# Optimization experiments

Hardware: AMD Instinct MI355X
Metric: run time of the kernel (lower is better)

Reference implementation:

```python
import jax, jax.numpy as jnp
import numpy as np

EPS = 1e-5


def _corner_data(x, cmin, stride, D, H, W):
    # continuous grid indices (x_idx, y_idx, z_idx); index 0 = first voxel center
    idx = (x - cmin[None, :]) / stride[None, :]
    gx, gy, gz = idx[:, 0], idx[:, 1], idx[:, 2]
    x0 = jnp.floor(gx); y0 = jnp.floor(gy); z0 = jnp.floor(gz)
    fx = jnp.clip(gx - x0, 0.0, 1.0)
    fy = jnp.clip(gy - y0, 0.0, 1.0)
    fz = jnp.clip(gz - z0, 0.0, 1.0)
    x0i = x0.astype(jnp.int32); x1i = x0i + 1
    y0i = y0.astype(jnp.int32); y1i = y0i + 1
    z0i = z0.astype(jnp.int32); z1i = z0i + 1
    # 8 trilinear corners, same order as the torch reference
    xs = jnp.stack([x0i, x1i, x0i, x1i, x0i, x1i, x0i, x1i])
    ys = jnp.stack([y0i, y0i, y1i, y1i, y0i, y0i, y1i, y1i])
    zs = jnp.stack([z0i, z0i, z0i, z0i, z1i, z1i, z1i, z1i])
    wx = jnp.stack([1 - fx, fx, 1 - fx, fx, 1 - fx, fx, 1 - fx, fx])
    wy = jnp.stack([1 - fy, 1 - fy, fy, fy, 1 - fy, 1 - fy, fy, fy])
    wz = jnp.stack([1 - fz, 1 - fz, 1 - fz, 1 - fz, fz, fz, fz, fz])
    ws = wx * wy * wz                                    # (8, N)
    valid = (xs >= 0) & (xs < W) & (ys >= 0) & (ys < H) & (zs >= 0) & (zs < D)
    xi = jnp.clip(xs, 0, W - 1)
    yi = jnp.clip(ys, 0, H - 1)
    zi = jnp.clip(zs, 0, D - 1)
    flat = zi * (H * W) + yi * W + xi                    # (8, N) flat voxel index
    return flat, ws * valid.astype(ws.dtype)


def setup_inputs() -> dict:
    key = jax.random.key(0)
    ks = jax.random.split(key, 20)
    N = 200000; B = 4; D = H = W = 64; CG = 64; NC = 128; HID = 128
    h = jax.random.normal(ks[0], (N, NC), jnp.float32)
    x = jax.random.uniform(ks[1], (N, 3), jnp.float32) * 63.0
    grid = jax.random.normal(ks[2], (B, CG, D, H, W), jnp.float32)
    node_batch = jax.random.randint(ks[3], (N,), 0, B, jnp.int32)
    coordinates_min = jnp.zeros((3,), jnp.float32)
    spatial_stride = jnp.ones((3,), jnp.float32)
    s = 0.05
    params = dict(
        w1=jax.random.normal(ks[4], (HID, NC + CG), jnp.float32) * s,
        b1=jax.random.normal(ks[5], (HID,), jnp.float32) * s,
        w2=jax.random.normal(ks[6], (NC, HID), jnp.float32) * s,
        b2=jax.random.normal(ks[7], (NC,), jnp.float32) * s,
        ln_g=1.0 + jax.random.normal(ks[8], (NC,), jnp.float32) * s,
        ln_b=jax.random.normal(ks[9], (NC,), jnp.float32) * s,
        wn2g=jax.random.normal(ks[10], (CG, NC), jnp.float32) * s,
        bn2g=jax.random.normal(ks[11], (CG,), jnp.float32) * s,
        wc1=jax.random.normal(ks[12], (CG, 2 * CG), jnp.float32) * s,
        bc1=jax.random.normal(ks[13], (CG,), jnp.float32) * s,
        wc2=jax.random.normal(ks[14], (CG, CG), jnp.float32) * s,
        bc2=jax.random.normal(ks[15], (CG,), jnp.float32) * s,
        in_g=1.0 + jax.random.normal(ks[16], (CG,), jnp.float32) * s,
        in_b=jax.random.normal(ks[17], (CG,), jnp.float32) * s,
    )
    return dict(h=h, x=x, grid=grid, node_batch=node_batch,
                coordinates_min=coordinates_min, spatial_stride=spatial_stride, **params)


def reference(h, x, grid, node_batch, coordinates_min, spatial_stride,
              w1, b1, w2, b2, ln_g, ln_b, wn2g, bn2g, wc1, bc1, wc2, bc2, in_g, in_b):
    B, Cg, D, H, W = grid.shape
    DHW = D * H * W
    flat, w = _corner_data(x, coordinates_min, spatial_stride, D, H, W)  # (8,N)

    # grid -> node: trilinear gather (== grid_sample, align_corners=True, zeros padding)
    gflat = grid.reshape(B, Cg, DHW).transpose(0, 2, 1)                  # (B,DHW,Cg)
    vals = gflat[node_batch[None, :], flat]                              # (8,N,Cg)
    sampled = jnp.einsum('kn,knc->nc', w, vals)                          # (N,Cg)

    # node MLP + residual + LayerNorm
    z = jnp.concatenate([h, sampled], axis=-1)
    m = jax.nn.silu(z @ w1.T + b1) @ w2.T + b2
    hn = h + m
    mu = hn.mean(-1, keepdims=True)
    var = hn.var(-1, keepdims=True)
    hn = (hn - mu) / jnp.sqrt(var + EPS) * ln_g + ln_b

    # node -> grid: trilinear scatter-add splat of projected features
    proj = hn @ wn2g.T + bn2g                                            # (N,Cg)
    gidx = node_batch[None, :] * DHW + flat                              # (8,N) global flat index
    contrib = w[:, :, None] * proj[None]                                 # (8,N,Cg)
    vol = jnp.zeros((B * DHW, Cg), grid.dtype).at[gidx.reshape(-1)].add(contrib.reshape(-1, Cg))
    splat = vol.reshape(B, D, H, W, Cg).transpose(0, 4, 1, 2, 3)         # (B,Cg,D,H,W)

    # grid MLP (1x1x1 convs) + residual + InstanceNorm (affine)
    cat = jnp.concatenate([grid, splat], axis=1)                         # (B,2Cg,D,H,W)
    g1 = jax.nn.silu(jnp.einsum('bcdhw,oc->bodhw', cat, wc1) + bc1[None, :, None, None, None])
    g2 = jnp.einsum('bcdhw,oc->bodhw', g1, wc2) + bc2[None, :, None, None, None]
    gr = grid + g2
    mu = gr.mean((2, 3, 4), keepdims=True)
    var = gr.var((2, 3, 4), keepdims=True)
    gr = (gr - mu) / jnp.sqrt(var + EPS) * in_g[None, :, None, None, None] + in_b[None, :, None, None, None]
    return hn, gr
```

## Files before the change

### kernel.cpp

```cpp
#include <hip/hip_runtime.h>
#include <hip/hip_fp16.h>
#include <cstdint>

#define NNODES 200000
#define NCH 128
#define NBATCH 4
#define DHW 262144
#define K1 192

#define VOLH_OFF  0ull
#define VOLH_BYTES 134217728ull
#define PART_OFF  134217728ull
#define STAT_OFF  142606336ull
#define NWF_OFF   142608384ull
#define WF_OFF    142706688ull
#define GT_OFF    257931264ull
#define GRH_OFF   392149056ull

typedef _Float16 h2 __attribute__((ext_vector_type(2)));
typedef __fp16  fp16x2 __attribute__((ext_vector_type(2)));
typedef _Float16 f16x8 __attribute__((ext_vector_type(8)));
typedef float f32x4 __attribute__((ext_vector_type(4)));

__device__ __forceinline__ uint32_t pack_h2(float a, float b){
  fp16x2 p = __builtin_amdgcn_cvt_pkrtz(a, b);
  return __builtin_bit_cast(uint32_t, p);
}
__device__ __forceinline__ h2 as_h2(uint32_t w){ return __builtin_bit_cast(h2, w); }
__device__ __forceinline__ float siluf(float a){ return a / (1.f + __expf(-a)); }
__device__ __forceinline__ f32x4 mfma16(uint4 a, uint4 b, f32x4 c){
  return __builtin_amdgcn_mfma_f32_16x16x32_f16(
      __builtin_bit_cast(f16x8, a), __builtin_bit_cast(f16x8, b), c, 0, 0, 0);
}
__device__ __forceinline__ void atomic_pk_add_f16(uint32_t* addr, uint32_t val){
  asm volatile("global_atomic_pk_add_f16 %0, %1, off"
               :: "v"(addr), "v"(val) : "memory");
}

__global__ void fill_kernel(uint4* __restrict__ p, size_t n4)
{
  size_t stride = (size_t)gridDim.x * 256;
  const uint4 z = make_uint4(0u, 0u, 0u, 0u);
  for (size_t i = blockIdx.x * 256 + threadIdx.x; i < n4; i += stride) p[i] = z;
}

__global__ void pack_all(const float* __restrict__ w1, const float* __restrict__ w2,
                         const float* __restrict__ wn2g,
                         const float* __restrict__ wc1, const float* __restrict__ wc2,
                         uint32_t* __restrict__ nwf, uint32_t* __restrict__ wf)
{
  int t = blockIdx.x * 256 + threadIdx.x;
  if (t < 24576) {
    int q = t & 3, lane = (t >> 2) & 63;
    int vl = lane & 15, g = lane >> 4;
    if (t < 12288) {
      int f = t >> 8, s = f % 6, tt = f / 6;
      int o = tt * 16 + vl, k = s * 32 + g * 8 + 2 * q;
      nwf[t] = pack_h2(w1[o * K1 + k], w1[o * K1 + k + 1]);
    } else if (t < 20480) {
      int f = (t - 12288) >> 8, s = f & 3, tt = f >> 2;
      int o = tt * 16 + vl, k = s * 32 + g * 8 + 2 * q;
      nwf[t] = pack_h2(w2[o * 128 + k], w2[o * 128 + k + 1]);
    } else {
      int f = (t - 20480) >> 8, s = f & 3, tt = f >> 2;
      int o = tt * 16 + vl, k = s * 32 + g * 8 + 2 * q;
      nwf[t] = pack_h2(wn2g[o * 128 + k], wn2g[o * 128 + k + 1]);
    }
  } else if (t < 30720) {
    int u = t - 24576;
    if (u < 4096) {
      int q = u & 3, lane = (u >> 2) & 63, f = u >> 8;
      int s = f & 3, tt = f >> 2;
      int o = tt * 16 + (lane & 15);
      int k = s * 32 + (lane >> 4) * 8 + 2 * q;
      wf[u] = pack_h2(wc1[o * 128 + k], wc1[o * 128 + k + 1]);
    } else {
      int uu = u - 4096;
      int q = uu & 3, lane = (uu >> 2) & 63, f = uu >> 8;
      int s = f & 1, tt = f >> 1;
      int o = tt * 16 + (lane & 15);
      int k = s * 32 + (lane >> 4) * 8 + 2 * q;
      wf[u] = pack_h2(wc2[o * 64 + k], wc2[o * 64 + k + 1]);
    }
  }
}

__global__ void transpose_kernel(const float* __restrict__ grid, uint32_t* __restrict__ gt)
{
  __shared__ float tile[64][65];
  int bx = blockIdx.x;
  int b = bx >> 12;
  int dhw0 = (bx & 4095) << 6;
  const float* gbase = grid + ((size_t)b * 64) * DHW + dhw0;
  int c0 = threadIdx.x >> 6, d = threadIdx.x & 63;
  #pragma unroll
  for (int i = 0; i < 16; ++i)
    tile[i * 4 + c0][d] = gbase[(size_t)(i * 4 + c0) * DHW + d];
  __syncthreads();
  uint32_t* tb = gt + ((size_t)b * DHW + dhw0) * 32;
  int p = threadIdx.x & 31, r0 = threadIdx.x >> 5;
  #pragma unroll
  for (int i = 0; i < 8; ++i) {
    int dd = i * 8 + r0;
    tb[(size_t)dd * 32 + p] = pack_h2(tile[2 * p][dd], tile[2 * p + 1][dd]);
  }
}

__launch_bounds__(256, 2)
__global__ void node_fused(const float* __restrict__ h, const float* __restrict__ x,
                           const uint32_t* __restrict__ gridT, const int* __restrict__ nbat,
                           const float* __restrict__ cmin, const float* __restrict__ sstr,
                           const uint32_t* __restrict__ nwf,
                           const float* __restrict__ b1, const float* __restrict__ b2,
                           const float* __restrict__ ln_g, const float* __restrict__ ln_b,
                           const float* __restrict__ bn2g,
                           float* __restrict__ hn_out, uint32_t* __restrict__ volh)
{
  __shared__ __align__(16) uint32_t zt[64][100];
  __shared__ __align__(16) uint32_t g1z[64][68];
  __shared__ float wpart[4][64][2];
  __shared__ float cwS[64][8];
  __shared__ int   cfS[64][8];

  const int tid = threadIdx.x;
  const int lane = tid & 63, w = tid >> 6;
  const int g = lane >> 4, vl = lane & 15;
  const int n0 = blockIdx.x * 64;

  {
    const float c0 = cmin[0], c1 = cmin[1], c2 = cmin[2];
    const float st0 = sstr[0], st1 = sstr[1], st2 = sstr[2];
    int nd = tid & 63, j = tid >> 6;
    int n = n0 + nd;
    float gx = (x[n * 3 + 0] - c0) / st0;
    float gy = (x[n * 3 + 1] - c1) / st1;
    float gz = (x[n * 3 + 2] - c2) / st2;
    float fx0 = floorf(gx), fy0 = floorf(gy), fz0 = floorf(gz);
    float fx = fminf(fmaxf(gx - fx0, 0.f), 1.f);
    float fy = fminf(fmaxf(gy - fy0, 0.f), 1.f);
    float fz = fminf(fmaxf(gz - fz0, 0.f), 1.f);
    int ix0 = (int)fx0, iy0 = (int)fy0, iz0 = (int)fz0;
    int b = nbat[n];
    #pragma unroll
    for (int kk = 0; kk < 2; ++kk) {
      int k = 2 * j + kk;
      int xi = (k & 1) ? ix0 + 1 : ix0;
      int yi = (k & 2) ? iy0 + 1 : iy0;
      int zi = (k & 4) ? iz0 + 1 : iz0;
      float wx = (k & 1) ? fx : 1.f - fx;
      float wy = (k & 2) ? fy : 1.f - fy;
      float wz = (k & 4) ? fz : 1.f - fz;
      bool valid = (xi >= 0) & (xi < 64) & (yi >= 0) & (yi < 64) & (zi >= 0) & (zi < 64);
      int xc = min(max(xi, 0), 63), yc = min(max(yi, 0), 63), zc = min(max(zi, 0), 63);
      cwS[nd][k] = valid ? wx * wy * wz : 0.f;
      cfS[nd][k] = b * DHW + ((zc << 12) | (yc << 6) | xc);
    }
  }
  {
    int nd = tid >> 2, q = tid & 3;
    const float4* hp = (const float4*)&h[(size_t)(n0 + nd) * NCH + q * 32];
    #pragma unroll
    for (int r = 0; r < 8; ++r) {
      float4 f = hp[r];
      zt[nd][q * 16 + 2 * r]     = pack_h2(f.x, f.y);
      zt[nd][q * 16 + 2 * r + 1] = pack_h2(f.z, f.w);
    }
  }
  __syncthreads();

  {
    const int p = lane & 31, kb = lane >> 5;
    #pragma unroll 4
    for (int i = 0; i < 16; ++i) {
      int nd = w * 16 + i;
      float slo = 0.f, shi = 0.f;
      #pragma unroll
      for (int jj = 0; jj < 4; ++jj) {
        int k = 2 * jj + kb;
        int   cfk = cfS[nd][k];
        float cwk = cwS[nd][k];
        h2 gv = as_h2(gridT[(size_t)cfk * 32 + p]);
        slo = fmaf(cwk, (float)gv.x, slo);
        shi = fmaf(cwk, (float)gv.y, shi);
      }
      slo += __shfl_xor(slo, 32);
      shi += __shfl_xor(shi, 32);
      if (lane < 32) zt[nd][64 + p] = pack_h2(slo, shi);
    }
  }
  __syncthreads();

  const uint4* nf4 = (const uint4*)nwf;
  uint4 a1f[2][6], a2f[2][4], apf[4];
  #pragma unroll
  for (int j = 0; j < 2; ++j) {
    int tt = 2 * w + j;
    #pragma unroll
    for (int s = 0; s < 6; ++s) a1f[j][s] = nf4[(tt * 6 + s) * 64 + lane];
    #pragma unroll
    for (int s = 0; s < 4; ++s) a2f[j][s] = nf4[3072 + (tt * 4 + s) * 64 + lane];
  }
  #pragma unroll
  for (int s = 0; s < 4; ++s) apf[s] = nf4[5120 + (w * 4 + s) * 64 + lane];

  float4 b1r[2], b2r[2], lgr[2], lbr[2], bnr;
  #pragma unroll
  for (int j = 0; j < 2; ++j) {
    int c = (2 * w + j) * 16 + g * 4;
    b1r[j] = *(const float4*)&b1[c];
    b2r[j] = *(const float4*)&b2[c];
    lgr[j] = *(const float4*)&ln_g[c];
    lbr[j] = *(const float4*)&ln_b[c];
  }
  bnr = *(const float4*)&bn2g[w * 16 + g * 4];

  #pragma unroll
  for (int nc = 0; nc < 4; ++nc) {
    uint4 bfr[6];
    #pragma unroll
    for (int s = 0; s < 6; ++s) bfr[s] = *(const uint4*)&zt[nc * 16 + vl][s * 16 + g * 4];
    f32x4 acc[2];
    acc[0][0]=b1r[0].x; acc[0][1]=b1r[0].y; acc[0][2]=b1r[0].z; acc[0][3]=b1r[0].w;
    acc[1][0]=b1r[1].x; acc[1][1]=b1r[1].y; acc[1][2]=b1r[1].z; acc[1][3]=b1r[1].w;
    #pragma unroll
    for (int s = 0; s < 6; ++s) {
      acc[0] = mfma16(a1f[0][s], bfr[s], acc[0]);
      acc[1] = mfma16(a1f[1][s], bfr[s], acc[1]);
    }
    #pragma unroll
    for (int j = 0; j < 2; ++j) {
      uint2 pr;
      pr.x = pack_h2(siluf(acc[j][0]), siluf(acc[j][1]));
      pr.y = pack_h2(siluf(acc[j][2]), siluf(acc[j][3]));
      *(uint2*)&g1z[nc * 16 + vl][(2 * w + j) * 8 + g * 2] = pr;
    }
  }
  __syncthreads();

  float hnv[2][4][4];
  #pragma unroll
  for (int nc = 0; nc < 4; ++nc) {
    uint4 bfr[4];
    #pragma unroll
    for (int s = 0; s < 4; ++s) bfr[s] = *(const uint4*)&g1z[nc * 16 + vl][s * 16 + g * 4];
    f32x4 acc[2];
    acc[0][0]=b2r[0].x; acc[0][1]=b2r[0].y; acc[0][2]=b2r[0].z; acc[0][3]=b2r[0].w;
    acc[1][0]=b2r[1].x; acc[1][1]=b2r[1].y; acc[1][2]=b2r[1].z; acc[1][3]=b2r[1].w;
    #pragma unroll
    for (int s = 0; s < 4; ++s) {
      acc[0] = mfma16(a2f[0][s], bfr[s], acc[0]);
      acc[1] = mfma16(a2f[1][s], bfr[s], acc[1]);
    }
    float s_ = 0.f, q_ = 0.f;
    #pragma unroll
    for (int j = 0; j < 2; ++j) {
      uint2 hp = *(const uint2*)&zt[nc * 16 + vl][(2 * w + j) * 8 + g * 2];
      h2 p0 = as_h2(hp.x), p1 = as_h2(hp.y);
      float v0 = acc[j][0] + (float)p0.x;
      float v1 = acc[j][1] + (float)p0.y;
      float v2 = acc[j][2] + (float)p1.x;
      float v3 = acc[j][3] + (float)p1.y;
      hnv[j][nc][0] = v0; hnv[j][nc][1] = v1; hnv[j][nc][2] = v2; hnv[j][nc][3] = v3;
      s_ += v0 + v1 + v2 + v3;
      q_ += v0 * v0 + v1 * v1 + v2 * v2 + v3 * v3;
    }
    s_ += __shfl_xor(s_, 16); q_ += __shfl_xor(q_, 16);
    s_ += __shfl_xor(s_, 32); q_ += __shfl_xor(q_, 32);
    if (lane < 16) { wpart[w][nc * 16 + lane][0] = s_; wpart[w][nc * 16 + lane][1] = q_; }
  }
  __syncthreads();

  #pragma unroll
  for (int nc = 0; nc < 4; ++nc) {
    int node = nc * 16 + vl;
    float2 p0 = *(const float2*)&wpart[0][node][0];
    float2 p1 = *(const float2*)&wpart[1][node][0];
    float2 p2 = *(const float2*)&wpart[2][node][0];
    float2 p3 = *(const float2*)&wpart[3][node][0];
    float mu = (p0.x + p1.x + p2.x + p3.x) * (1.f / 128.f);
    float var = (p0.y + p1.y + p2.y + p3.y) * (1.f / 128.f) - mu * mu;
    float rstd = rsqrtf(var + 1e-5f);
    #pragma unroll
    for (int j = 0; j < 2; ++j) {
      float y0 = (hnv[j][nc][0] - mu) * rstd * ((const float*)&lgr[j])[0] + ((const float*)&lbr[j])[0];
      float y1 = (hnv[j][nc][1] - mu) * rstd * ((const float*)&lgr[j])[1] + ((const float*)&lbr[j])[1];
      float y2 = (hnv[j][nc][2] - mu) * rstd * ((const float*)&lgr[j])[2] + ((const float*)&lbr[j])[2];
      float y3 = (hnv[j][nc][3] - mu) * rstd * ((const float*)&lgr[j])[3] + ((const float*)&lbr[j])[3];
      *(float4*)&hn_out[(size_t)(n0 + node) * NCH + (2 * w + j) * 16 + g * 4] =
          make_float4(y0, y1, y2, y3);
      uint2 pz;
      pz.x = pack_h2(y0, y1);
      pz.y = pack_h2(y2, y3);
      *(uint2*)&g1z[node][(2 * w + j) * 8 + g * 2] = pz;
    }
  }
  __syncthreads();

  #pragma unroll
  for (int nc = 0; nc < 4; ++nc) {
    int node = nc * 16 + vl;
    uint4 bfr[4];
    #pragma unroll
    for (int s = 0; s < 4; ++s) bfr[s] = *(const uint4*)&g1z[node][s * 16 + g * 4];
    f32x4 acc;
    acc[0]=bnr.x; acc[1]=bnr.y; acc[2]=bnr.z; acc[3]=bnr.w;
    #pragma unroll
    for (int s = 0; s < 4; ++s) acc = mfma16(apf[s], bfr[s], acc);
    uint2 pr;
    pr.x = pack_h2(acc[0], acc[1]);
    pr.y = pack_h2(acc[2], acc[3]);
    *(uint2*)&zt[node][w * 8 + g * 2] = pr;
  }
  __syncthreads();

  {
    const int half = lane >> 5, c = lane & 31;
    for (int i = 0; i < 16; ++i) {
      int node = w * 16 + i;
      uint32_t pz = zt[node][c];
      h2 p = as_h2(pz);
      #pragma unroll
      for (int kk = 0; kk < 4; ++kk) {
        int k = 2 * kk + half;
        float wv = cwS[node][k];
        if (wv != 0.f) {
          int gidx = cfS[node][k];
          uint32_t v = pack_h2(wv * (float)p.x, wv * (float)p.y);
          atomic_pk_add_f16(&volh[(size_t)gidx * 32 + c], v);
        }
      }
    }
  }
}

__launch_bounds__(256, 2)
__global__ void voxel_kernel(const uint32_t* __restrict__ gridT, const uint32_t* __restrict__ volh,
                             const uint32_t* __restrict__ wf, const float* __restrict__ bc1,
                             const float* __restrict__ bc2,
                             _Float16* __restrict__ grh, float* __restrict__ partials)
{
  __shared__ __align__(16) uint32_t xt[64][68];
  __shared__ __align__(16) uint32_t g1b[4][16][36];
  __shared__ float part_s[4][128];

  const int tid = threadIdx.x;
  const int lane = tid & 63, wv = tid >> 6;
  const int g = lane >> 4, vl = lane & 15;
  const int b = blockIdx.x >> 12;
  const int dhw0 = (blockIdx.x & 4095) << 6;

  {
    const uint32_t* gt = gridT + ((size_t)b * DHW + dhw0) * 32;
    #pragma unroll
    for (int it = 0; it < 2; ++it) {
      int u = it * 256 + tid;
      int v = u >> 3, p4 = u & 7;
      *(uint4*)&xt[v][4 * p4] = *(const uint4*)&gt[(size_t)v * 32 + 4 * p4];
    }
  }
  {
    const uint32_t* vb = volh + ((size_t)b * DHW + dhw0) * 32;
    #pragma unroll
    for (int it = 0; it < 2; ++it) {
      int u = it * 256 + tid;
      int v = u >> 3, p4 = u & 7;
      *(uint4*)&xt[v][32 + 4 * p4] = *(const uint4*)&vb[(size_t)v * 32 + 4 * p4];
    }
  }

  const uint4* wf4 = (const uint4*)wf;
  uint4 w1f[4][4], w2f[4][2];
  #pragma unroll
  for (int t = 0; t < 4; ++t)
    #pragma unroll
    for (int s = 0; s < 4; ++s)
      w1f[t][s] = wf4[(t * 4 + s) * 64 + lane];
  #pragma unroll
  for (int t = 0; t < 4; ++t)
    #pragma unroll
    for (int s = 0; s < 2; ++s)
      w2f[t][s] = wf4[1024 + (t * 2 + s) * 64 + lane];

  f32x4 acc1[4];
  #pragma unroll
  for (int t = 0; t < 4; ++t) {
    #pragma unroll
    for (int r = 0; r < 4; ++r) acc1[t][r] = bc1[t * 16 + g * 4 + r];
  }

  __syncthreads();

  const int v = wv * 16 + vl;
  #pragma unroll
  for (int s = 0; s < 4; ++s) {
    uint4 xb = *(const uint4*)&xt[v][s * 16 + g * 4];
    #pragma unroll
    for (int t = 0; t < 4; ++t) acc1[t] = mfma16(w1f[t][s], xb, acc1[t]);
  }

  #pragma unroll
  for (int t = 0; t < 4; ++t) {
    uint2 pr;
    pr.x = pack_h2(siluf(acc1[t][0]), siluf(acc1[t][1]));
    pr.y = pack_h2(siluf(acc1[t][2]), siluf(acc1[t][3]));
    *(uint2*)&g1b[wv][vl][t * 8 + g * 2] = pr;
  }
  asm volatile("s_waitcnt lgkmcnt(0)" ::: "memory");

  f32x4 acc2[4];
  #pragma unroll
  for (int t = 0; t < 4; ++t) {
    #pragma unroll
    for (int r = 0; r < 4; ++r) acc2[t][r] = bc2[t * 16 + g * 4 + r];
  }
  #pragma unroll
  for (int s = 0; s < 2; ++s) {
    uint4 gv = *(const uint4*)&g1b[wv][vl][s * 16 + g * 4];
    #pragma unroll
    for (int t = 0; t < 4; ++t) acc2[t] = mfma16(w2f[t][s], gv, acc2[t]);
  }

  const int dhw = dhw0 + v;
  #pragma unroll
  for (int t = 0; t < 4; ++t) {
    uint2 gp = *(const uint2*)&xt[v][t * 8 + g * 2];
    h2 g0 = as_h2(gp.x), g1 = as_h2(gp.y);
    float gc[4] = {(float)g0.x, (float)g0.y, (float)g1.x, (float)g1.y};
    #pragma unroll
    for (int r = 0; r < 4; ++r) {
      int o = t * 16 + g * 4 + r;
      float grv = gc[r] + acc2[t][r];
      grh[(size_t)(b * 64 + o) * DHW + dhw] = (_Float16)grv;
      float sv = grv, qv = grv * grv;
      sv += __shfl_xor(sv, 1, 64); qv += __shfl_xor(qv, 1, 64);
      sv += __shfl_xor(sv, 2, 64); qv += __shfl_xor(qv, 2, 64);
      sv += __shfl_xor(sv, 4, 64); qv += __shfl_xor(qv, 4, 64);
      sv += __shfl_xor(sv, 8, 64); qv += __shfl_xor(qv, 8, 64);
      if (vl == 0) { part_s[wv][2 * o] = sv; part_s[wv][2 * o + 1] = qv; }
    }
  }
  __syncthreads();
  if (tid < 128)
    partials[(size_t)blockIdx.x * 128 + tid] =
        part_s[0][tid] + part_s[1][tid] + part_s[2][tid] + part_s[3][tid];
}

__global__ void stats_kernel(const float* __restrict__ partials, const float* __restrict__ in_g,
                             const float* __restrict__ in_b, float* __restrict__ stats)
{
  int bo = blockIdx.x;
  int b = bo >> 6, o = bo & 63;
  float s = 0.f, q = 0.f;
  for (int k = threadIdx.x; k < 4096; k += 256) {
    const float* pp = partials + (size_t)(b * 4096 + k) * 128 + 2 * o;
    s += pp[0]; q += pp[1];
  }
  __shared__ float sred[256], qred[256];
  sred[threadIdx.x] = s; qred[threadIdx.x] = q;
  __syncthreads();
  for (int st = 128; st >= 1; st >>= 1) {
    if (threadIdx.x < st) { sred[threadIdx.x] += sred[threadIdx.x + st]; qred[threadIdx.x] += qred[threadIdx.x + st]; }
    __syncthreads();
  }
  if (threadIdx.x == 0) {
    float mu = sred[0] * (1.f / (float)DHW);
    float var = qred[0] * (1.f / (float)DHW) - mu * mu;
    float rstd = rsqrtf(var + 1e-5f);
    float scale = rstd * in_g[o];
    stats[2 * bo] = scale;
    stats[2 * bo + 1] = in_b[o] - mu * scale;
  }
}

__global__ void norm_kernel(const uint2* __restrict__ grh2, const float* __restrict__ stats,
                            float* __restrict__ gr)
{
  const size_t total = (size_t)NBATCH * 64 * DHW / 4;
  size_t stride = (size_t)gridDim.x * 256;
  for (size_t i = blockIdx.x * 256 + threadIdx.x; i < total; i += stride) {
    int bo = (int)(i >> 16);
    float scale = stats[2 * bo], shift = stats[2 * bo + 1];
    uint2 u = grh2[i];
    h2 p0 = as_h2(u.x), p1 = as_h2(u.y);
    float4 o;
    o.x = fmaf((float)p0.x, scale, shift);
    o.y = fmaf((float)p0.y, scale, shift);
    o.z = fmaf((float)p1.x, scale, shift);
    o.w = fmaf((float)p1.y, scale, shift);
    *(float4*)&gr[4 * i] = o;
  }
}

extern "C" void kernel_launch(void* const* d_in, const int* in_sizes, int n_in,
                              void* d_out, int out_size, void* d_ws, size_t ws_size,
                              hipStream_t stream)
{
  const float* h     = (const float*)d_in[0];
  const float* x     = (const float*)d_in[1];
  const float* grid  = (const float*)d_in[2];
  const int*   nbat  = (const int*)d_in[3];
  const float* cmin  = (const float*)d_in[4];
  const float* sstr  = (const float*)d_in[5];
  const float* w1    = (const float*)d_in[6];
  const float* b1    = (const float*)d_in[7];
  const float* w2    = (const float*)d_in[8];
  const float* b2    = (const float*)d_in[9];
  const float* ln_g  = (const float*)d_in[10];
  const float* ln_b  = (const float*)d_in[11];
  const float* wn2g  = (const float*)d_in[12];
  const float* bn2g  = (const float*)d_in[13];
  const float* wc1   = (const float*)d_in[14];
  const float* bc1   = (const float*)d_in[15];
  const float* wc2   = (const float*)d_in[16];
  const float* bc2   = (const float*)d_in[17];
  const float* in_g  = (const float*)d_in[18];
  const float* in_b  = (const float*)d_in[19];

  float* hn_out = (float*)d_out;
  float* gr_out = (float*)d_out + (size_t)NNODES * NCH;

  char* ws = (char*)d_ws;
  uint32_t* volh     = (uint32_t*)(ws + VOLH_OFF);
  float*    partials = (float*)(ws + PART_OFF);
  float*    stats    = (float*)(ws + STAT_OFF);
  uint32_t* nwf      = (uint32_t*)(ws + NWF_OFF);
  uint32_t* wf       = (uint32_t*)(ws + WF_OFF);
  uint32_t* gridT    = (uint32_t*)(ws + GT_OFF);
  _Float16* grh      = (_Float16*)(ws + GRH_OFF);

  fill_kernel<<<2048, 256, 0, stream>>>((uint4*)volh, VOLH_BYTES / 16);
  pack_all<<<120, 256, 0, stream>>>(w1, w2, wn2g, wc1, wc2, nwf, wf);
  transpose_kernel<<<16384, 256, 0, stream>>>(grid, gridT);
  node_fused<<<3125, 256, 0, stream>>>(h, x, gridT, nbat, cmin, sstr, nwf,
                                       b1, b2, ln_g, ln_b, bn2g, hn_out, volh);
  voxel_kernel<<<16384, 256, 0, stream>>>(gridT, volh, wf, bc1, bc2, grh, partials);
  stats_kernel<<<256, 256, 0, stream>>>(partials, in_g, in_b, stats);
  norm_kernel<<<8192, 256, 0, stream>>>((const uint2*)grh, stats, gr_out);
}
```

Baseline: 603.3 us.

## Fold volume zeroing into transpose and widen node kernel to 512 threads

The separate fill kernel is removed, and the fp16 splat volume is now zeroed inside transpose_kernel. Each of its 16384 blocks writes 512 uint4, which covers the full 128 MiB, so one launch and one extra pass over memory are saved. node_fused now runs 8 wavefronts per block instead of 4. Each wave owns one 16-channel output tile instead of two, so it holds fewer MFMA weight fragments in registers, and the gather, scatter and load phases are spread over more threads. The costs are the launch bound moving from (256,2) to (512,1), eight per-wave partial sums for the LayerNorm reduction, and the projection matmul split across wave halves.

Result: faster. 589.9 us (-2.2%).

```diff
diff --git a/kernel.cpp b/kernel.cpp
--- a/kernel.cpp
+++ b/kernel.cpp
@@ -35,13 +35,6 @@
 __device__ __forceinline__ void atomic_pk_add_f16(uint32_t* addr, uint32_t val){
   asm volatile("global_atomic_pk_add_f16 %0, %1, off"
                :: "v"(addr), "v"(val) : "memory");
-}
-
-__global__ void fill_kernel(uint4* __restrict__ p, size_t n4)
-{
-  size_t stride = (size_t)gridDim.x * 256;
-  const uint4 z = make_uint4(0u, 0u, 0u, 0u);
-  for (size_t i = blockIdx.x * 256 + threadIdx.x; i < n4; i += stride) p[i] = z;
 }
 
 __global__ void pack_all(const float* __restrict__ w1, const float* __restrict__ w2,
@@ -85,9 +78,16 @@
   }
 }
 
-__global__ void transpose_kernel(const float* __restrict__ grid, uint32_t* __restrict__ gt)
+__global__ void transpose_kernel(const float* __restrict__ grid, uint32_t* __restrict__ gt,
+                                 uint4* __restrict__ volz)
 {
   __shared__ float tile[64][65];
+  {
+    size_t base = (size_t)blockIdx.x * 512 + threadIdx.x;
+    const uint4 z = make_uint4(0u, 0u, 0u, 0u);
+    volz[base] = z;
+    volz[base + 256] = z;
+  }
   int bx = blockIdx.x;
   int b = bx >> 12;
   int dhw0 = (bx & 4095) << 6;
@@ -106,7 +106,7 @@
   }
 }
 
-__launch_bounds__(256, 2)
+__launch_bounds__(512, 1)
 __global__ void node_fused(const float* __restrict__ h, const float* __restrict__ x,
                            const uint32_t* __restrict__ gridT, const int* __restrict__ nbat,
                            const float* __restrict__ cmin, const float* __restrict__ sstr,
@@ -118,7 +118,7 @@
 {
   __shared__ __align__(16) uint32_t zt[64][100];
   __shared__ __align__(16) uint32_t g1z[64][68];
-  __shared__ float wpart[4][64][2];
+  __shared__ float wpart[8][64][2];
   __shared__ float cwS[64][8];
   __shared__ int   cfS[64][8];
 
@@ -127,10 +127,26 @@
   const int g = lane >> 4, vl = lane & 15;
   const int n0 = blockIdx.x * 64;
 
+  const uint4* nf4 = (const uint4*)nwf;
+  uint4 a1f[6], a2f[4], apf[4];
+  #pragma unroll
+  for (int s = 0; s < 6; ++s) a1f[s] = nf4[(w * 6 + s) * 64 + lane];
+  #pragma unroll
+  for (int s = 0; s < 4; ++s) a2f[s] = nf4[3072 + (w * 4 + s) * 64 + lane];
+  #pragma unroll
+  for (int s = 0; s < 4; ++s) apf[s] = nf4[5120 + ((w & 3) * 4 + s) * 64 + lane];
+
+  const int cbase = w * 16 + g * 4;
+  float4 b1r = *(const float4*)&b1[cbase];
+  float4 b2r = *(const float4*)&b2[cbase];
+  float4 lgr = *(const float4*)&ln_g[cbase];
+  float4 lbr = *(const float4*)&ln_b[cbase];
+  float4 bnr = *(const float4*)&bn2g[(w & 3) * 16 + g * 4];
+
   {
     const float c0 = cmin[0], c1 = cmin[1], c2 = cmin[2];
     const float st0 = sstr[0], st1 = sstr[1], st2 = sstr[2];
-    int nd = tid & 63, j = tid >> 6;
+    int nd = tid & 63, k = tid >> 6;
     int n = n0 + nd;
     float gx = (x[n * 3 + 0] - c0) / st0;
     float gy = (x[n * 3 + 1] - c1) / st1;
@@ -141,29 +157,25 @@
     float fz = fminf(fmaxf(gz - fz0, 0.f), 1.f);
     int ix0 = (int)fx0, iy0 = (int)fy0, iz0 = (int)fz0;
     int b = nbat[n];
-    #pragma unroll
-    for (int kk = 0; kk < 2; ++kk) {
-      int k = 2 * j + kk;
-      int xi = (k & 1) ? ix0 + 1 : ix0;
-      int yi = (k & 2) ? iy0 + 1 : iy0;
-      int zi = (k & 4) ? iz0 + 1 : iz0;
-      float wx = (k & 1) ? fx : 1.f - fx;
-      float wy = (k & 2) ? fy : 1.f - fy;
-      float wz = (k & 4) ? fz : 1.f - fz;
-      bool valid = (xi >= 0) & (xi < 64) & (yi >= 0) & (yi < 64) & (zi >= 0) & (zi < 64);
-      int xc = min(max(xi, 0), 63), yc = min(max(yi, 0), 63), zc = min(max(zi, 0), 63);
-      cwS[nd][k] = valid ? wx * wy * wz : 0.f;
-      cfS[nd][k] = b * DHW + ((zc << 12) | (yc << 6) | xc);
-    }
-  }
-  {
-    int nd = tid >> 2, q = tid & 3;
-    const float4* hp = (const float4*)&h[(size_t)(n0 + nd) * NCH + q * 32];
-    #pragma unroll
-    for (int r = 0; r < 8; ++r) {
-      float4 f = hp[r];
-      zt[nd][q * 16 + 2 * r]     = pack_h2(f.x, f.y);
-      zt[nd][q * 16 + 2 * r + 1] = pack_h2(f.z, f.w);
+    int xi = (k & 1) ? ix0 + 1 : ix0;
+    int yi = (k & 2) ? iy0 + 1 : iy0;
+    int zi = (k & 4) ? iz0 + 1 : iz0;
+    float wx = (k & 1) ? fx : 1.f - fx;
+    float wy = (k & 2) ? fy : 1.f - fy;
+    float wz = (k & 4) ? fz : 1.f - fz;
+    bool valid = (xi >= 0) & (xi < 64) & (yi >= 0) & (yi < 64) & (zi >= 0) & (zi < 64);
+    int xc = min(max(xi, 0), 63), yc = min(max(yi, 0), 63), zc = min(max(zi, 0), 63);
+    cwS[nd][k] = valid ? wx * wy * wz : 0.f;
+    cfS[nd][k] = b * DHW + ((zc << 12) | (yc << 6) | xc);
+  }
+  {
+    int nd = tid >> 3, o = tid & 7;
+    const float4* hp = (const float4*)&h[(size_t)(n0 + nd) * NCH + o * 16];
+    #pragma unroll
+    for (int u = 0; u < 4; ++u) {
+      float4 f = hp[u];
+      zt[nd][o * 8 + 2 * u]     = pack_h2(f.x, f.y);
+      zt[nd][o * 8 + 2 * u + 1] = pack_h2(f.z, f.w);
     }
   }
   __syncthreads();
@@ -171,8 +183,8 @@
   {
     const int p = lane & 31, kb = lane >> 5;
     #pragma unroll 4
-    for (int i = 0; i < 16; ++i) {
-      int nd = w * 16 + i;
+    for (int i = 0; i < 8; ++i) {
+      int nd = w * 8 + i;
       float slo = 0.f, shi = 0.f;
       #pragma unroll
       for (int jj = 0; jj < 4; ++jj) {
@@ -190,80 +202,41 @@
   }
   __syncthreads();
 
-  const uint4* nf4 = (const uint4*)nwf;
-  uint4 a1f[2][6], a2f[2][4], apf[4];
-  #pragma unroll
-  for (int j = 0; j < 2; ++j) {
-    int tt = 2 * w + j;
-    #pragma unroll
-    for (int s = 0; s < 6; ++s) a1f[j][s] = nf4[(tt * 6 + s) * 64 + lane];
-    #pragma unroll
-    for (int s = 0; s < 4; ++s) a2f[j][s] = nf4[3072 + (tt * 4 + s) * 64 + lane];
-  }
-  #pragma unroll
-  for (int s = 0; s < 4; ++s) apf[s] = nf4[5120 + (w * 4 + s) * 64 + lane];
-
-  float4 b1r[2], b2r[2], lgr[2], lbr[2], bnr;
-  #pragma unroll
-  for (int j = 0; j < 2; ++j) {
-    int c = (2 * w + j) * 16 + g * 4;
-    b1r[j] = *(const float4*)&b1[c];
-    b2r[j] = *(const float4*)&b2[c];
-    lgr[j] = *(const float4*)&ln_g[c];
-    lbr[j] = *(const float4*)&ln_b[c];
-  }
-  bnr = *(const float4*)&bn2g[w * 16 + g * 4];
-
   #pragma unroll
   for (int nc = 0; nc < 4; ++nc) {
     uint4 bfr[6];
     #pragma unroll
     for (int s = 0; s < 6; ++s) bfr[s] = *(const uint4*)&zt[nc * 16 + vl][s * 16 + g * 4];
-    f32x4 acc[2];
-    acc[0][0]=b1r[0].x; acc[0][1]=b1r[0].y; acc[0][2]=b1r[0].z; acc[0][3]=b1r[0].w;
-    acc[1][0]=b1r[1].x; acc[1][1]=b1r[1].y; acc[1][2]=b1r[1].z; acc[1][3]=b1r[1].w;
-    #pragma unroll
-    for (int s = 0; s < 6; ++s) {
-      acc[0] = mfma16(a1f[0][s], bfr[s], acc[0]);
-      acc[1] = mfma16(a1f[1][s], bfr[s], acc[1]);
-    }
-    #pragma unroll
-    for (int j = 0; j < 2; ++j) {
-      uint2 pr;
-      pr.x = pack_h2(siluf(acc[j][0]), siluf(acc[j][1]));
-      pr.y = pack_h2(siluf(acc[j][2]), siluf(acc[j][3]));
-      *(uint2*)&g1z[nc * 16 + vl][(2 * w + j) * 8 + g * 2] = pr;
-    }
-  }
-  __syncthreads();
-
-  float hnv[2][4][4];
+    f32x4 acc;
+    acc[0] = b1r.x; acc[1] = b1r.y; acc[2] = b1r.z; acc[3] = b1r.w;
+    #pragma unroll
+    for (int s = 0; s < 6; ++s) acc = mfma16(a1f[s], bfr[s], acc);
+    uint2 pr;
+    pr.x = pack_h2(siluf(acc[0]), siluf(acc[1]));
+    pr.y = pack_h2(siluf(acc[2]), siluf(acc[3]));
+    *(uint2*)&g1z[nc * 16 + vl][w * 8 + g * 2] = pr;
+  }
+  __syncthreads();
+
+  float hnv[4][4];
   #pragma unroll
   for (int nc = 0; nc < 4; ++nc) {
     uint4 bfr[4];
     #pragma unroll
     for (int s = 0; s < 4; ++s) bfr[s] = *(const uint4*)&g1z[nc * 16 + vl][s * 16 + g * 4];
-    f32x4 acc[2];
-    acc[0][0]=b2r[0].x; acc[0][1]=b2r[0].y; acc[0][2]=b2r[0].z; acc[0][3]=b2r[0].w;
-    acc[1][0]=b2r[1].x; acc[1][1]=b2r[1].y; acc[1][2]=b2r[1].z; acc[1][3]=b2r[1].w;
-    #pragma unroll
-    for (int s = 0; s < 4; ++s) {
-      acc[0] = mfma16(a2f[0][s], bfr[s], acc[0]);
-      acc[1] = mfma16(a2f[1][s], bfr[s], acc[1]);
-    }
-    float s_ = 0.f, q_ = 0.f;
-    #pragma unroll
-    for (int j = 0; j < 2; ++j) {
-      uint2 hp = *(const uint2*)&zt[nc * 16 + vl][(2 * w + j) * 8 + g * 2];
-      h2 p0 = as_h2(hp.x), p1 = as_h2(hp.y);
-      float v0 = acc[j][0] + (float)p0.x;
-      float v1 = acc[j][1] + (float)p0.y;
-      float v2 = acc[j][2] + (float)p1.x;
-      float v3 = acc[j][3] + (float)p1.y;
-      hnv[j][nc][0] = v0; hnv[j][nc][1] = v1; hnv[j][nc][2] = v2; hnv[j][nc][3] = v3;
-      s_ += v0 + v1 + v2 + v3;
-      q_ += v0 * v0 + v1 * v1 + v2 * v2 + v3 * v3;
-    }
+    f32x4 acc;
+    acc[0] = b2r.x; acc[1] = b2r.y; acc[2] = b2r.z; acc[3] = b2r.w;
+    #pragma unroll
+    for (int s = 0; s < 4; ++s) acc = mfma16(a2f[s], bfr[s], acc);
+    uint2 hp = *(const uint2*)&zt[nc * 16 + vl][w * 8 + g * 2];
+    h2 p0 = as_h2(hp.x), p1 = as_h2(hp.y);
+    float v0 = acc[0] + (float)p0.x;
+    float v1 = acc[1] + (float)p0.y;
+    float v2 = acc[2] + (float)p1.x;
+    float v3 = acc[3] + (float)p1.y;
+    hnv[nc][0] = v0; hnv[nc][1] = v1; hnv[nc][2] = v2; hnv[nc][3] = v3;
+    float s_ = v0 + v1 + v2 + v3;
+    float q_ = v0 * v0 + v1 * v1 + v2 * v2 + v3 * v3;
     s_ += __shfl_xor(s_, 16); q_ += __shfl_xor(q_, 16);
     s_ += __shfl_xor(s_, 32); q_ += __shfl_xor(q_, 32);
     if (lane < 16) { wpart[w][nc * 16 + lane][0] = s_; wpart[w][nc * 16 + lane][1] = q_; }
@@ -273,50 +246,49 @@
   #pragma unroll
   for (int nc = 0; nc < 4; ++nc) {
     int node = nc * 16 + vl;
-    float2 p0 = *(const float2*)&wpart[0][node][0];
-    float2 p1 = *(const float2*)&wpart[1][node][0];
-    float2 p2 = *(const float2*)&wpart[2][node][0];
-    float2 p3 = *(const float2*)&wpart[3][node][0];
-    float mu = (p0.x + p1.x + p2.x + p3.x) * (1.f / 128.f);
-    float var = (p0.y + p1.y + p2.y + p3.y) * (1.f / 128.f) - mu * mu;
+    float ssum = 0.f, qsum = 0.f;
+    #pragma unroll
+    for (int ww = 0; ww < 8; ++ww) {
+      float2 pp = *(const float2*)&wpart[ww][node][0];
+      ssum += pp.x; qsum += pp.y;
+    }
+    float mu = ssum * (1.f / 128.f);
+    float var = qsum * (1.f / 128.f) - mu * mu;
     float rstd = rsqrtf(var + 1e-5f);
-    #pragma unroll
-    for (int j = 0; j < 2; ++j) {
-      float y0 = (hnv[j][nc][0] - mu) * rstd * ((const float*)&lgr[j])[0] + ((const float*)&lbr[j])[0];
-      float y1 = (hnv[j][nc][1] - mu) * rstd * ((const float*)&lgr[j])[1] + ((const float*)&lbr[j])[1];
-      float y2 = (hnv[j][nc][2] - mu) * rstd * ((const float*)&lgr[j])[2] + ((const float*)&lbr[j])[2];
-      float y3 = (hnv[j][nc][3] - mu) * rstd * ((const float*)&lgr[j])[3] + ((const float*)&lbr[j])[3];
-      *(float4*)&hn_out[(size_t)(n0 + node) * NCH + (2 * w + j) * 16 + g * 4] =
-          make_float4(y0, y1, y2, y3);
-      uint2 pz;
-      pz.x = pack_h2(y0, y1);
-      pz.y = pack_h2(y2, y3);
-      *(uint2*)&g1z[node][(2 * w + j) * 8 + g * 2] = pz;
-    }
-  }
-  __syncthreads();
-
-  #pragma unroll
-  for (int nc = 0; nc < 4; ++nc) {
+    float y0 = (hnv[nc][0] - mu) * rstd * lgr.x + lbr.x;
+    float y1 = (hnv[nc][1] - mu) * rstd * lgr.y + lbr.y;
+    float y2 = (hnv[nc][2] - mu) * rstd * lgr.z + lbr.z;
+    float y3 = (hnv[nc][3] - mu) * rstd * lgr.w + lbr.w;
+    *(float4*)&hn_out[(size_t)(n0 + node) * NCH + cbase] = make_float4(y0, y1, y2, y3);
+    uint2 pz;
+    pz.x = pack_h2(y0, y1);
+    pz.y = pack_h2(y2, y3);
+    *(uint2*)&g1z[node][w * 8 + g * 2] = pz;
+  }
+  __syncthreads();
+
+  #pragma unroll
+  for (int ncq = 0; ncq < 2; ++ncq) {
+    int nc = (w >> 2) * 2 + ncq;
     int node = nc * 16 + vl;
     uint4 bfr[4];
     #pragma unroll
     for (int s = 0; s < 4; ++s) bfr[s] = *(const uint4*)&g1z[node][s * 16 + g * 4];
     f32x4 acc;
-    acc[0]=bnr.x; acc[1]=bnr.y; acc[2]=bnr.z; acc[3]=bnr.w;
+    acc[0] = bnr.x; acc[1] = bnr.y; acc[2] = bnr.z; acc[3] = bnr.w;
     #pragma unroll
     for (int s = 0; s < 4; ++s) acc = mfma16(apf[s], bfr[s], acc);
     uint2 pr;
     pr.x = pack_h2(acc[0], acc[1]);
     pr.y = pack_h2(acc[2], acc[3]);
-    *(uint2*)&zt[node][w * 8 + g * 2] = pr;
+    *(uint2*)&zt[node][(w & 3) * 8 + g * 2] = pr;
   }
   __syncthreads();
 
   {
     const int half = lane >> 5, c = lane & 31;
-    for (int i = 0; i < 16; ++i) {
-      int node = w * 16 + i;
+    for (int i = 0; i < 8; ++i) {
+      int node = w * 8 + i;
       uint32_t pz = zt[node][c];
       h2 p = as_h2(pz);
       #pragma unroll
@@ -528,10 +500,9 @@
   uint32_t* gridT    = (uint32_t*)(ws + GT_OFF);
   _Float16* grh      = (_Float16*)(ws + GRH_OFF);
 
-  fill_kernel<<<2048, 256, 0, stream>>>((uint4*)volh, VOLH_BYTES / 16);
   pack_all<<<120, 256, 0, stream>>>(w1, w2, wn2g, wc1, wc2, nwf, wf);
-  transpose_kernel<<<16384, 256, 0, stream>>>(grid, gridT);
-  node_fused<<<3125, 256, 0, stream>>>(h, x, gridT, nbat, cmin, sstr, nwf,
+  transpose_kernel<<<16384, 256, 0, stream>>>(grid, gridT, (uint4*)volh);
+  node_fused<<<3125, 512, 0, stream>>>(h, x, gridT, nbat, cmin, sstr, nwf,
                                        b1, b2, ln_g, ln_b, bn2g, hn_out, volh);
   voxel_kernel<<<16384, 256, 0, stream>>>(gridT, volh, wf, bc1, bc2, grh, partials);
   stats_kernel<<<256, 256, 0, stream>>>(partials, in_g, in_b, stats);
```
